# Kernel optimization log

Hardware: AMD Instinct MI355X
Metric: run time of the kernel (lower is better)

## Reference

```python
import jax, jax.numpy as jnp
import numpy as np

L, H, R, N, E = 6, 128, 64, 10000, 160000
SSILU_SCALE = 1.0 / 0.6  # ScaledSiLU
INV_SQRT_3 = 1.0 / np.sqrt(3.0)
INV_SQRT_H = 1.0 / np.sqrt(H)
INV_SQRT_2 = 1.0 / np.sqrt(2.0)


def ssilu(x):
    return jax.nn.silu(x) * SSILU_SCALE


def lnorm(x, w, b):
    m = x.mean(-1, keepdims=True)
    v = jnp.var(x, axis=-1, keepdims=True)
    return (x - m) * jax.lax.rsqrt(v + 1e-5) * w + b


def gated_block(x, v, wv1, wv2, wu1, bu1, wu2, bu2, hout):
    # GatedEquivariantBlock: x [N,Hin], v [N,3,Hin]
    vec1 = jnp.linalg.norm(jnp.einsum('nci,io->nco', v, wv1), axis=-2)  # [N,Hin]
    vec2 = jnp.einsum('nci,io->nco', v, wv2)                            # [N,3,hout]
    h = ssilu(jnp.concatenate([x, vec1], -1) @ wu1 + bu1) @ wu2 + bu2   # [N,2*hout]
    xs, xv = h[..., :hout], h[..., hout:]
    return ssilu(xs), xv[:, None, :] * vec2


def forward_impl(edge_index, x, vec, edge_rbf, edge_vector,
                 ln_w, ln_b, xp1_w, xp1_b, xp2_w, xp2_b, rbf_w, rbf_b,
                 vp_w, xv1_w, xv1_b, xv2_w, xv2_b,
                 we1, be1, we2, be2,
                 g1_v1, g1_v2, g1_u1, g1_u1b, g1_u2, g1_u2b,
                 g2_v1, g2_v2, g2_u1, g2_u1b, g2_u2, g2_u2b):
    src, dst = edge_index[0], edge_index[1]  # message flows src(j) -> dst(i)
    for l in range(L):
        # ---- PaiNNMessage ----
        xh = ssilu(lnorm(x, ln_w[l], ln_b[l]) @ xp1_w[l] + xp1_b[l]) @ xp2_w[l] + xp2_b[l]  # [N,3H]
        rbfh = edge_rbf @ rbf_w[l] + rbf_b[l]                                                # [E,3H]
        m = xh[src] * rbfh                                                                    # gather + elementwise
        mx = m[:, :H]
        m2 = m[:, H:2 * H] * INV_SQRT_3
        m3 = m[:, 2 * H:]
        mvec = (vec[src] * m2[:, None, :] + m3[:, None, :] * edge_vector[:, :, None]) * INV_SQRT_H  # [E,3,H]
        dx = jax.ops.segment_sum(mx, dst, num_segments=N)
        dvec = jax.ops.segment_sum(mvec, dst, num_segments=N)
        x = (x + dx) * INV_SQRT_2
        vec = vec + dvec
        # ---- PaiNNUpdate ----
        vp = jnp.einsum('nci,io->nco', vec, vp_w[l])  # [N,3,2H]
        v1, v2 = vp[..., :H], vp[..., H:]
        vec_dot = (v1 * v2).sum(axis=1) * INV_SQRT_H  # [N,H]
        vnorm = jnp.sqrt((v2 ** 2).sum(axis=-2) + 1e-8)
        h = ssilu(jnp.concatenate([x, vnorm], -1) @ xv1_w[l] + xv1_b[l]) @ xv2_w[l] + xv2_b[l]  # [N,3H]
        xu1, xu2, xu3 = h[:, :H], h[:, H:2 * H], h[:, 2 * H:]
        x = x + (xu1 + xu2 * vec_dot) * INV_SQRT_2
        vec = vec + xu3[:, None, :] * v1
        # ScaleFactor is identity without a scale file
    energy = ssilu(x @ we1 + be1) @ we2 + be2  # [N,1] per-atom energy
    fx, fv = gated_block(x, vec, g1_v1, g1_v2, g1_u1, g1_u1b, g1_u2, g1_u2b, H // 2)
    fx, fv = gated_block(fx, fv, g2_v1, g2_v2, g2_u1, g2_u1b, g2_u2, g2_u2b, 1)
    forces = fv[..., 0]  # [N,3]
    return jnp.concatenate([energy, forces], axis=-1)  # [N,4] packed (energy, fx, fy, fz)


def setup_inputs() -> dict:
    key = jax.random.key(0)
    ks = iter(jax.random.split(key, 64))
    nrm = lambda shape, s=0.05: jax.random.normal(next(ks), shape, jnp.float32) * s
    return dict(
        x=jax.random.normal(next(ks), (N, H), jnp.float32),
        vec=jax.random.normal(next(ks), (N, 3, H), jnp.float32),
        edge_index=jax.random.randint(next(ks), (2, E), 0, N),
        edge_rbf=jax.random.uniform(next(ks), (E, R), jnp.float32),
        edge_vector=jax.random.normal(next(ks), (E, 3), jnp.float32),
        ln_w=jnp.ones((L, H)), ln_b=jnp.zeros((L, H)),
        xp1_w=nrm((L, H, H)), xp1_b=jnp.zeros((L, H)),
        xp2_w=nrm((L, H, 3 * H)), xp2_b=jnp.zeros((L, 3 * H)),
        rbf_w=nrm((L, R, 3 * H)), rbf_b=jnp.zeros((L, 3 * H)),
        vp_w=nrm((L, H, 2 * H)),
        xv1_w=nrm((L, 2 * H, H)), xv1_b=jnp.zeros((L, H)),
        xv2_w=nrm((L, H, 3 * H)), xv2_b=jnp.zeros((L, 3 * H)),
        we1=nrm((H, H // 2)), be1=jnp.zeros((H // 2,)),
        we2=nrm((H // 2, 1)), be2=jnp.zeros((1,)),
        g1_v1=nrm((H, H)), g1_v2=nrm((H, H // 2)),
        g1_u1=nrm((2 * H, H)), g1_u1b=jnp.zeros((H,)),
        g1_u2=nrm((H, H)), g1_u2b=jnp.zeros((H,)),
        g2_v1=nrm((H // 2, H // 2)), g2_v2=nrm((H // 2, 1)),
        g2_u1=nrm((H, H // 2)), g2_u1b=jnp.zeros((H // 2,)),
        g2_u2=nrm((H // 2, 2)), g2_u2b=jnp.zeros((2,)),
    )


def reference(x, vec, edge_index, edge_rbf, edge_vector,
              ln_w, ln_b, xp1_w, xp1_b, xp2_w, xp2_b, rbf_w, rbf_b,
              vp_w, xv1_w, xv1_b, xv2_w, xv2_b,
              we1, be1, we2, be2,
              g1_v1, g1_v2, g1_u1, g1_u1b, g1_u2, g1_u2b,
              g2_v1, g2_v2, g2_u1, g2_u1b, g2_u2, g2_u2b):
    return forward_impl(edge_index, x, vec, edge_rbf, edge_vector,
                        ln_w, ln_b, xp1_w, xp1_b, xp2_w, xp2_b, rbf_w, rbf_b,
                        vp_w, xv1_w, xv1_b, xv2_w, xv2_b,
                        we1, be1, we2, be2,
                        g1_v1, g1_v2, g1_u1, g1_u1b, g1_u2, g1_u2b,
                        g2_v1, g2_v2, g2_u1, g2_u1b, g2_u2, g2_u2b)
```

## Files before the change

kernel.cpp:

```cpp
#include <hip/hip_runtime.h>
#include <hip/hip_bf16.h>

#define NN 10000
#define EE 160000
#define LL 6

#define INV_SQRT_3f  0.57735026919f
#define INV_SQRT_Hf  0.08838834764832f
#define INV_SQRT_2f  0.70710678118655f

typedef _Float16 half8 __attribute__((ext_vector_type(8)));
typedef float f32x4 __attribute__((ext_vector_type(4)));

__device__ __forceinline__ float ssilu_f(float v){
  float s = 1.0f / (1.0f + __expf(-v));
  return v * s * 1.6666666666667f;
}
__device__ __forceinline__ float bcast(float v, int l){
  return __int_as_float(__builtin_amdgcn_readlane(__float_as_int(v), l));
}

__global__ __launch_bounds__(256) void k_hist(const int* __restrict__ edst, int* __restrict__ cnt){
  int i = blockIdx.x*256 + threadIdx.x;
  if (i < EE) atomicAdd(&cnt[edst[i]], 1);
}

__global__ __launch_bounds__(1024) void k_scan(const int* __restrict__ cnt,
                                               int* __restrict__ off, int* __restrict__ cur){
  __shared__ int ps[1024];
  int t = threadIdx.x;
  int base = t*10;
  int local[10];
  int s = 0;
  #pragma unroll
  for (int i=0;i<10;i++){
    int c = (base+i < NN) ? cnt[base+i] : 0;
    local[i] = s; s += c;
  }
  ps[t] = s;
  __syncthreads();
  for (int d=1; d<1024; d<<=1){
    int v = (t>=d) ? ps[t-d] : 0;
    __syncthreads();
    ps[t] += v;
    __syncthreads();
  }
  int pre = (t>0) ? ps[t-1] : 0;
  #pragma unroll
  for (int i=0;i<10;i++){
    int idx = base+i;
    if (idx < NN){ int o = pre + local[i]; off[idx]=o; cur[idx]=o; }
  }
  if (t==1023) off[NN] = ps[1023];
}

__global__ __launch_bounds__(256) void k_fill(const int* __restrict__ edst,
                                              int* __restrict__ cur, int* __restrict__ eord){
  int i = blockIdx.x*256 + threadIdx.x;
  if (i < EE){
    int d = edst[i];
    int p = atomicAdd(&cur[d], 1);
    eord[p] = i;
  }
}

__global__ __launch_bounds__(256) void k_packw(const float* __restrict__ w, _Float16* __restrict__ wf){
  int i = blockIdx.x*256 + threadIdx.x;
  if (i >= LL*24*2*64*8) return;
  int j    = i & 7;
  int lane = (i >> 3) & 63;
  int kh   = (i >> 9) & 1;
  int rest = i >> 10;
  int nb   = rest % 24;
  int l    = rest / 24;
  int k    = 32*kh + 8*(lane>>4) + j;
  int ch   = nb*16 + (lane&15);
  float v = w[((size_t)l*64 + k)*384 + ch];
  if (ch >= 128 && ch < 256) v *= INV_SQRT_3f;
  wf[i] = (_Float16)v;
}

__global__ __launch_bounds__(256) void k_packb(const float* __restrict__ b, float* __restrict__ bsc){
  int i = blockIdx.x*256 + threadIdx.x;
  if (i >= LL*384) return;
  int ch = i % 384;
  float v = b[i];
  if (ch >= 128 && ch < 256) v *= INV_SQRT_3f;
  bsc[i] = v;
}

struct PackTab {
  const float* s[30];
  _Float16* d[30];
  int K[30];
  int NO[30];
};
__global__ __launch_bounds__(256) void k_packall(PackTab tb){
  int e = blockIdx.y;
  int K = tb.K[e], NO = tb.NO[e];
  int tot = K*NO, KS = K >> 5;
  const float* s = tb.s[e];
  _Float16* d = tb.d[e];
  for (int i = blockIdx.x*256 + threadIdx.x; i < tot; i += gridDim.x*256){
    int j = i & 7, lane = (i >> 3) & 63, rest = i >> 9;
    int ks = rest % KS, nb = rest / KS;
    int k = ks*32 + (lane>>4)*8 + j, n = nb*16 + (lane&15);
    d[i] = (_Float16)s[(size_t)k*NO + n];
  }
}

__global__ __launch_bounds__(256) void k_cvt16(const float* __restrict__ v, _Float16* __restrict__ o, int n){
  int i = blockIdx.x*256 + threadIdx.x;
  if (i < n) o[i] = (_Float16)v[i];
}

__global__ __launch_bounds__(64) void k_gemm_rbfh(
    const float* __restrict__ erbf, const _Float16* __restrict__ wf,
    const float* __restrict__ bsc, const int* __restrict__ eord,
    _Float16* __restrict__ rbfh)
{
  int lane = threadIdx.x;
  int i0 = blockIdx.x * 64;
  int ml = lane & 15, kg = lane >> 4;
  half8 a0[4], a1[4];
  #pragma unroll
  for (int tt = 0; tt < 4; tt++){
    int e_m = eord[i0 + tt*16 + ml];
    const float* ar = erbf + (size_t)e_m*64 + 8*kg;
    float4 p0 = *(const float4*)(ar);
    float4 p1 = *(const float4*)(ar+4);
    a0[tt][0]=(_Float16)p0.x; a0[tt][1]=(_Float16)p0.y; a0[tt][2]=(_Float16)p0.z; a0[tt][3]=(_Float16)p0.w;
    a0[tt][4]=(_Float16)p1.x; a0[tt][5]=(_Float16)p1.y; a0[tt][6]=(_Float16)p1.z; a0[tt][7]=(_Float16)p1.w;
    float4 p2 = *(const float4*)(ar+32);
    float4 p3 = *(const float4*)(ar+36);
    a1[tt][0]=(_Float16)p2.x; a1[tt][1]=(_Float16)p2.y; a1[tt][2]=(_Float16)p2.z; a1[tt][3]=(_Float16)p2.w;
    a1[tt][4]=(_Float16)p3.x; a1[tt][5]=(_Float16)p3.y; a1[tt][6]=(_Float16)p3.z; a1[tt][7]=(_Float16)p3.w;
  }
  #pragma unroll 2
  for (int nb = 0; nb < 24; nb++){
    half8 b0 = *(const half8*)(wf + ((size_t)(nb*2+0)*64 + lane)*8);
    half8 b1 = *(const half8*)(wf + ((size_t)(nb*2+1)*64 + lane)*8);
    float bias = bsc[nb*16 + ml];
    #pragma unroll
    for (int tt = 0; tt < 4; tt++){
      f32x4 acc = {bias, bias, bias, bias};
      acc = __builtin_amdgcn_mfma_f32_16x16x32_f16(a0[tt], b0, acc, 0, 0, 0);
      acc = __builtin_amdgcn_mfma_f32_16x16x32_f16(a1[tt], b1, acc, 0, 0, 0);
      _Float16* orow = rbfh + (size_t)(i0 + tt*16)*384 + nb*16 + ml;
      #pragma unroll
      for (int r = 0; r < 4; r++)
        orow[(size_t)(kg*4 + r)*384] = (_Float16)acc[r];
    }
  }
}

__global__ __launch_bounds__(256) void k_xh_mfma(
    const float* __restrict__ x,
    const float* __restrict__ lnw, const float* __restrict__ lnb,
    const _Float16* __restrict__ wf1, const float* __restrict__ b1,
    const _Float16* __restrict__ wf2, const float* __restrict__ b2,
    _Float16* __restrict__ xh16)
{
  __shared__ _Float16 sA[32][136];
  __shared__ _Float16 sH[32][136];
  int t = threadIdx.x;
  int n0 = blockIdx.x * 32;
  {
    int nd = t >> 3, sb = t & 7;
    int node = n0 + nd;
// ... 52 lines not shown
      int nb = (w&1)*4 + nb4;
      #pragma unroll
      for (int r = 0; r < 4; r++)
        sH[mt*16 + kg*4 + r][nb*16 + ml] = (_Float16)hout[nb4][r];
    }
  }
  __syncthreads();
  {
    half8 a[4];
    #pragma unroll
    for (int ks = 0; ks < 4; ks++)
      a[ks] = *(const half8*)&sH[mt*16 + ml][ks*32 + kg*8];
    #pragma unroll 4
    for (int nb12 = 0; nb12 < 12; nb12++){
      int nb = (w&1)*12 + nb12;
      float bias = b2[nb*16 + ml];
      f32x4 acc = {bias, bias, bias, bias};
      #pragma unroll
      for (int ks = 0; ks < 4; ks++)
        acc = __builtin_amdgcn_mfma_f32_16x16x32_f16(a[ks],
                *(const half8*)(wf2 + ((size_t)(nb*4+ks)*64 + lane)*8), acc, 0,0,0);
      #pragma unroll
      for (int r = 0; r < 4; r++){
        int m = mt*16 + kg*4 + r;
        int node = n0 + m;
        if (node < NN) xh16[(size_t)node*384 + nb*16 + ml] = (_Float16)acc[r];
      }
    }
  }
}

__global__ __launch_bounds__(256) void k_edge3(
    const _Float16* __restrict__ rbfh,
    const int* __restrict__ esrc,
    const int* __restrict__ eord, const int* __restrict__ off,
    const float* __restrict__ evec,
    const _Float16* __restrict__ xh16, const _Float16* __restrict__ vec16,
    float* __restrict__ dx, float* __restrict__ dvec)
{
  int t = threadIdx.x;
  int lane = t & 63;
  int n = blockIdx.x*4 + (t>>6);
  if (n >= NN) return;
  int o0 = off[n], o1 = off[n+1];
  float ax0 = 0.f, ax1 = 0.f;
  float av00=0.f, av01=0.f, av10=0.f, av11=0.f, av20=0.f, av21=0.f;
  #pragma unroll 2
  for (int p = o0; p < o1; p++){
    int eid = eord[p];
    const _Float16* hr = rbfh + (size_t)p*384;
    float h0 = (float)hr[lane];
    float h1 = (float)hr[64+lane];
    float h2 = (float)hr[128+lane];
    float h3 = (float)hr[192+lane];
    float h4 = (float)hr[256+lane];
    float h5 = (float)hr[320+lane];
    int sN = esrc[eid];
    const _Float16* xr = xh16 + (size_t)sN*384;
    float m0  = h0 * (float)xr[lane];
    float m1  = h1 * (float)xr[64+lane];
    float m2a = h2 * (float)xr[128+lane];
    float m2b = h3 * (float)xr[192+lane];
    float m3a = h4 * (float)xr[256+lane];
    float m3b = h5 * (float)xr[320+lane];
    ax0 += m0; ax1 += m1;
    const _Float16* vr = vec16 + (size_t)sN*384;
    float ev0 = evec[(size_t)eid*3 + 0];
    float ev1 = evec[(size_t)eid*3 + 1];
    float ev2 = evec[(size_t)eid*3 + 2];
    av00 = fmaf((float)vr[lane],     m2a, av00); av00 = fmaf(m3a, ev0, av00);
    av01 = fmaf((float)vr[64+lane],  m2b, av01); av01 = fmaf(m3b, ev0, av01);
    av10 = fmaf((float)vr[128+lane], m2a, av10); av10 = fmaf(m3a, ev1, av10);
    av11 = fmaf((float)vr[192+lane], m2b, av11); av11 = fmaf(m3b, ev1, av11);
    av20 = fmaf((float)vr[256+lane], m2a, av20); av20 = fmaf(m3a, ev2, av20);
    av21 = fmaf((float)vr[320+lane], m2b, av21); av21 = fmaf(m3b, ev2, av21);
  }
  float* dxr = dx + (size_t)n*128;
  dxr[lane] = ax0; dxr[64+lane] = ax1;
  float* dvr = dvec + (size_t)n*384;
  dvr[lane]     = av00 * INV_SQRT_Hf;
  dvr[64+lane]  = av01 * INV_SQRT_Hf;
  dvr[128+lane] = av10 * INV_SQRT_Hf;
  dvr[192+lane] = av11 * INV_SQRT_Hf;
  dvr[256+lane] = av20 * INV_SQRT_Hf;
  dvr[320+lane] = av21 * INV_SQRT_Hf;
}

__global__ __launch_bounds__(256) void k_node_mfma(
    float* __restrict__ xbuf, float* __restrict__ vbuf,
    const float* __restrict__ dx, const float* __restrict__ dvec,
    const _Float16* __restrict__ wfvp,
    const _Float16* __restrict__ wfxv1, const float* __restrict__ xv1_b,
    const _Float16* __restrict__ wfxv2, const float* __restrict__ xv2_b,
    _Float16* __restrict__ vec16)
{
  __shared__ _Float16 sV1[96][136];
  __shared__ _Float16 sCat[32][264];
  __shared__ _Float16 sVD[32][128];
  int t = threadIdx.x;
  int n0 = blockIdx.x * 32;
  int lane = t & 63, w = t >> 6, ml = lane & 15, kg = lane >> 4;
  int mt = w & 1, nbb = (w >> 1) * 4;
  float vd[4][4], vn[4][4];
  #pragma unroll
  for (int i=0;i<4;i++){
    #pragma unroll
    for (int r=0;r<4;r++){ vd[i][r]=0.f; vn[i][r]=0.f; }
  }
// ... 114 lines not shown
      #pragma unroll
      for (int ks = 0; ks < 4; ks++){
        au1 = __builtin_amdgcn_mfma_f32_16x16x32_f16(a[ks],
                *(const half8*)(wfxv2 + ((size_t)(nbu*4+ks)*64 + lane)*8), au1, 0,0,0);
        au2 = __builtin_amdgcn_mfma_f32_16x16x32_f16(a[ks],
                *(const half8*)(wfxv2 + ((size_t)((nbu+8)*4+ks)*64 + lane)*8), au2, 0,0,0);
        au3 = __builtin_amdgcn_mfma_f32_16x16x32_f16(a[ks],
                *(const half8*)(wfxv2 + ((size_t)((nbu+16)*4+ks)*64 + lane)*8), au3, 0,0,0);
      }
      #pragma unroll
      for (int r = 0; r < 4; r++){
        int m = mt*16 + kg*4 + r;
        int node = n0 + m;
        if (node >= NN) continue;
        int c = nbu*16 + ml;
        float xu1 = au1[r], xu2 = au2[r], xu3 = au3[r];
        float vdv = (float)sVD[m][c];
        size_t px = (size_t)node*128 + c;
        float xn = (xbuf[px] + dx[px]) * INV_SQRT_2f;
        xbuf[px] = xn + (xu1 + xu2*vdv) * INV_SQRT_2f;
        #pragma unroll
        for (int cd = 0; cd < 3; cd++){
          float v1v = (float)sV1[cd*32 + m][c];
          size_t pv = (size_t)node*384 + cd*128 + c;
          float vo = vbuf[pv] + dvec[pv] + xu3*v1v;
          vbuf[pv] = vo;
          vec16[pv] = (_Float16)vo;
        }
      }
    }
  }
}

__global__ __launch_bounds__(256) void k_final1(
    const float* __restrict__ x, const float* __restrict__ vec,
    const float* __restrict__ we1, const float* __restrict__ be1,
    const float* __restrict__ we2, const float* __restrict__ be2,
    const float* __restrict__ wv1, const float* __restrict__ wv2,
    const float* __restrict__ wu1, const float* __restrict__ bu1,
    const float* __restrict__ wu2, const float* __restrict__ bu2,
    float* __restrict__ out, float* __restrict__ fx, float* __restrict__ fv)
{
  __shared__ __align__(16) float s_x[8][128];
  __shared__ __align__(16) float s_vl[8][384];
  __shared__ __align__(16) float s_p[8][384];
  __shared__ __align__(16) float s_n1[8][128];
  __shared__ __align__(16) float s_v2[8][192];
  __shared__ __align__(16) float s_h[8][128];
  __shared__ __align__(16) float s_h2[8][128];
  __shared__ __align__(16) float s_e1[8][64];
  int t = threadIdx.x;
  int n0 = blockIdx.x * 8;
  for (int idx = t; idx < 8*128; idx += 256){
    int i = idx >> 7, h = idx & 127;
    s_x[i][h] = x[(size_t)(n0+i)*128 + h];
  }
  for (int idx = t; idx < 8*384; idx += 256){
    int i = idx / 384, h = idx % 384;
    s_vl[i][h] = vec[(size_t)(n0+i)*384 + h];
  }
  __syncthreads();
  {
    int c = t & 63;
    int gb = t >> 6;
    #pragma unroll
    for (int u = 0; u < 2; u++){
      int i = gb + 4*u;
      float acc = be1[c];
      for (int k = 0; k < 128; k += 4){
        float w0 = we1[(k+0)*64+c], wq = we1[(k+1)*64+c], wz = we1[(k+2)*64+c], ww = we1[(k+3)*64+c];
        float4 a = *(const float4*)&s_x[i][k];
        acc = fmaf(a.x,w0,acc); acc=fmaf(a.y,wq,acc); acc=fmaf(a.z,wz,acc); acc=fmaf(a.w,ww,acc);
      }
      s_e1[i][c] = ssilu_f(acc);
    }
  }
  __syncthreads();
  {
    int lane = t & 63;
    int gb = t >> 6;
    #pragma unroll
    for (int u = 0; u < 2; u++){
      int i = gb + 4*u;
      float v = s_e1[i][lane] * we2[lane];
      #pragma unroll
      for (int off = 32; off > 0; off >>= 1) v += __shfl_xor(v, off, 64);
      if (lane == 0) out[(size_t)(n0+i)*4 + 0] = v + be2[0];
    }
  }
  {
    int ob = t & 127;
    int ib = (t >> 7) * 4;
    float acc[4][3];
    #pragma unroll
    for (int ii=0;ii<4;ii++){
      #pragma unroll
      for (int cd=0;cd<3;cd++) acc[ii][cd]=0.f;
    }
    for (int k = 0; k < 128; k += 4){
      float w0 = wv1[(k+0)*128+ob], wq=wv1[(k+1)*128+ob], wz=wv1[(k+2)*128+ob], ww=wv1[(k+3)*128+ob];
      #pragma unroll
      for (int ii=0;ii<4;ii++){
        #pragma unroll
        for (int cd=0;cd<3;cd++){
          float4 a = *(const float4*)&s_vl[ib+ii][cd*128+k];
          float s0=acc[ii][cd];
          s0=fmaf(a.x,w0,s0); s0=fmaf(a.y,wq,s0); s0=fmaf(a.z,wz,s0); s0=fmaf(a.w,ww,s0);
          acc[ii][cd]=s0;
        }
      }
    }
    #pragma unroll
    for (int ii=0;ii<4;ii++){
      #pragma unroll
      for (int cd=0;cd<3;cd++) s_p[ib+ii][cd*128+ob] = acc[ii][cd];
    }
  }
  __syncthreads();
  #pragma unroll
  for (int rep = 0; rep < 4; rep++){
    int idx = rep*256+t;
    int i = idx >> 7, h = idx & 127;
    float p0 = s_p[i][h], p1 = s_p[i][128+h], p2 = s_p[i][256+h];
    s_n1[i][h] = sqrtf(p0*p0 + p1*p1 + p2*p2);
  }
  {
    int c = t & 63;
    int gb = t >> 6;
    float acc[2][3];
    #pragma unroll
    for (int u=0;u<2;u++){
      #pragma unroll
      for (int cd=0;cd<3;cd++) acc[u][cd]=0.f;
    }
    for (int k=0;k<128;k+=4){
      float w0=wv2[(k+0)*64+c], wq=wv2[(k+1)*64+c], wz=wv2[(k+2)*64+c], ww=wv2[(k+3)*64+c];
      #pragma unroll
      for (int u=0;u<2;u++){
        int i = gb + 4*u;
        #pragma unroll
        for (int cd=0;cd<3;cd++){
          float4 a = *(const float4*)&s_vl[i][cd*128+k];
          float s0=acc[u][cd];
          s0=fmaf(a.x,w0,s0); s0=fmaf(a.y,wq,s0); s0=fmaf(a.z,wz,s0); s0=fmaf(a.w,ww,s0);
          acc[u][cd]=s0;
        }
      }
    }
    #pragma unroll
    for (int u=0;u<2;u++){
      int i=gb+4*u;
      #pragma unroll
      for (int cd=0;cd<3;cd++) s_v2[i][cd*64+c]=acc[u][cd];
    }
  }
  __syncthreads();
  {
    int c = t & 127;
    int ib = (t >> 7) * 4;
    float acc[4];
    float bv = bu1[c];
    #pragma unroll
    for (int ii=0;ii<4;ii++) acc[ii]=bv;
    for (int k=0;k<128;k+=4){
      float w0=wu1[(k+0)*128+c], wq=wu1[(k+1)*128+c], wz=wu1[(k+2)*128+c], ww=wu1[(k+3)*128+c];
      #pragma unroll
      for (int ii=0;ii<4;ii++){
        float4 a = *(const float4*)&s_x[ib+ii][k];
        acc[ii]=fmaf(a.x,w0,acc[ii]); acc[ii]=fmaf(a.y,wq,acc[ii]); acc[ii]=fmaf(a.z,wz,acc[ii]); acc[ii]=fmaf(a.w,ww,acc[ii]);
      }
    }
    for (int k=0;k<128;k+=4){
      float w0=wu1[(128+k+0)*128+c], wq=wu1[(128+k+1)*128+c], wz=wu1[(128+k+2)*128+c], ww=wu1[(128+k+3)*128+c];
      #pragma unroll
      for (int ii=0;ii<4;ii++){
        float4 a = *(const float4*)&s_n1[ib+ii][k];
        acc[ii]=fmaf(a.x,w0,acc[ii]); acc[ii]=fmaf(a.y,wq,acc[ii]); acc[ii]=fmaf(a.z,wz,acc[ii]); acc[ii]=fmaf(a.w,ww,acc[ii]);
      }
    }
    #pragma unroll
    for (int ii=0;ii<4;ii++) s_h[ib+ii][c] = ssilu_f(acc[ii]);
  }
  __syncthreads();
  {
    int c = t & 127;
    int ib = (t >> 7) * 4;
    float acc[4];
    float bv = bu2[c];
    #pragma unroll
    for (int ii=0;ii<4;ii++) acc[ii]=bv;
    for (int k=0;k<128;k+=4){
      float w0=wu2[(k+0)*128+c], wq=wu2[(k+1)*128+c], wz=wu2[(k+2)*128+c], ww=wu2[(k+3)*128+c];
      #pragma unroll
      for (int ii=0;ii<4;ii++){
        float4 a = *(const float4*)&s_h[ib+ii][k];
        acc[ii]=fmaf(a.x,w0,acc[ii]); acc[ii]=fmaf(a.y,wq,acc[ii]); acc[ii]=fmaf(a.z,wz,acc[ii]); acc[ii]=fmaf(a.w,ww,acc[ii]);
      }
    }
    #pragma unroll
    for (int ii=0;ii<4;ii++) s_h2[ib+ii][c] = acc[ii];
  }
  __syncthreads();
  {
    int c = t & 63;
    int gb = t >> 6;
    #pragma unroll
    for (int u=0;u<2;u++){
      int i = gb + 4*u;
      fx[(size_t)(n0+i)*64 + c] = ssilu_f(s_h2[i][c]);
      float xv = s_h2[i][64+c];
      #pragma unroll
      for (int cd=0;cd<3;cd++)
        fv[(size_t)(n0+i)*192 + cd*64 + c] = xv * s_v2[i][cd*64+c];
    }
  }
}

__global__ __launch_bounds__(256) void k_final2(
    const float* __restrict__ fx, const float* __restrict__ fv,
    const float* __restrict__ wv1, const float* __restrict__ wv2,
    const float* __restrict__ wu1, const float* __restrict__ bu1,
    const float* __restrict__ wu2, const float* __restrict__ bu2,
    float* __restrict__ out)
{
  int t = threadIdx.x;
  int lane = t & 63;
  int n = blockIdx.x * 4 + (t >> 6);
  float fxv = fx[(size_t)n*64 + lane];
  float f0 = fv[(size_t)n*192 + lane];
  float f1 = fv[(size_t)n*192 + 64 + lane];
  float f2 = fv[(size_t)n*192 + 128 + lane];
  float a0=0.f, a1=0.f, a2=0.f;
  for (int k=0;k<64;k++){
    float w = wv1[k*64 + lane];
    a0 = fmaf(bcast(f0,k), w, a0);
    a1 = fmaf(bcast(f1,k), w, a1);
    a2 = fmaf(bcast(f2,k), w, a2);
  }
  float n1 = sqrtf(a0*a0 + a1*a1 + a2*a2);
  float w2v = wv2[lane];
  float r0 = f0*w2v, r1 = f1*w2v, r2 = f2*w2v;
  #pragma unroll
  for (int off=32; off>0; off>>=1){
    r0 += __shfl_xor(r0, off, 64);
    r1 += __shfl_xor(r1, off, 64);
    r2 += __shfl_xor(r2, off, 64);
  }
  float acc = bu1[lane];
  for (int k=0;k<64;k++) acc = fmaf(bcast(fxv,k), wu1[k*64+lane], acc);
  for (int k=0;k<64;k++) acc = fmaf(bcast(n1,k), wu1[(64+k)*64+lane], acc);
  float hv = ssilu_f(acc);
  float s1 = hv * wu2[lane*2 + 1];
  #pragma unroll
  for (int off=32; off>0; off>>=1) s1 += __shfl_xor(s1, off, 64);
  float h2_1 = s1 + bu2[1];
  if (lane == 0){
    out[(size_t)n*4 + 1] = h2_1 * r0;
    out[(size_t)n*4 + 2] = h2_1 * r1;
    out[(size_t)n*4 + 3] = h2_1 * r2;
  }
}

extern "C" void kernel_launch(void* const* d_in, const int* in_sizes, int n_in,
                              void* d_out, int out_size, void* d_ws, size_t ws_size,
                              hipStream_t stream)
{
  const float* x_in   = (const float*)d_in[0];
  const float* vec_in = (const float*)d_in[1];
  const int*   eidx   = (const int*)d_in[2];
  const float* erbf   = (const float*)d_in[3];
  const float* evec   = (const float*)d_in[4];
  const float* ln_w  = (const float*)d_in[5];
  const float* ln_b  = (const float*)d_in[6];
  const float* xp1_w = (const float*)d_in[7];
  const float* xp1_b = (const float*)d_in[8];
  const float* xp2_w = (const float*)d_in[9];
  const float* xp2_b = (const float*)d_in[10];
  const float* rbf_w = (const float*)d_in[11];
  const float* rbf_b = (const float*)d_in[12];
  const float* vp_w  = (const float*)d_in[13];
  const float* xv1_w = (const float*)d_in[14];
  const float* xv1_b = (const float*)d_in[15];
  const float* xv2_w = (const float*)d_in[16];
  const float* xv2_b = (const float*)d_in[17];
  const float* we1 = (const float*)d_in[18];
  const float* be1 = (const float*)d_in[19];
  const float* we2 = (const float*)d_in[20];
  const float* be2 = (const float*)d_in[21];
  const float* g1_v1 = (const float*)d_in[22];
  const float* g1_v2 = (const float*)d_in[23];
  const float* g1_u1 = (const float*)d_in[24];
  const float* g1_u1b = (const float*)d_in[25];
  const float* g1_u2 = (const float*)d_in[26];
  const float* g1_u2b = (const float*)d_in[27];
  const float* g2_v1 = (const float*)d_in[28];
  const float* g2_v2 = (const float*)d_in[29];
  const float* g2_u1 = (const float*)d_in[30];
  const float* g2_u1b = (const float*)d_in[31];
  const float* g2_u2 = (const float*)d_in[32];
  const float* g2_u2b = (const float*)d_in[33];
  float* out = (float*)d_out;

  char* base = (char*)d_ws;
  size_t o = 0;
  auto alloc = [&](size_t bytes) -> char* {
    char* p = base + o;
    o = (o + bytes + 255) & ~(size_t)255;
    return p;
  };
  float* x_cur   = (float*)alloc((size_t)NN*128*4);
  float* vec_cur = (float*)alloc((size_t)NN*384*4);
  float* dx      = (float*)alloc((size_t)NN*128*4);
  float* dvec    = (float*)alloc((size_t)NN*384*4);
  _Float16* xh16 = (_Float16*)alloc((size_t)NN*384*2);
  _Float16* vec16= (_Float16*)alloc((size_t)NN*384*2);
  int*   eord    = (int*)alloc((size_t)EE*4);
  int*   off     = (int*)alloc((size_t)(NN+1)*4);
  _Float16* wf   = (_Float16*)alloc((size_t)LL*24576*2);
  float* bsc     = (float*)alloc((size_t)LL*384*4);
  _Float16* wfn  = (_Float16*)alloc((size_t)LL*180224*2);
  _Float16* rbfh = (_Float16*)alloc((size_t)EE*384*2);
  float* fxb = dx;
  float* fvb = dvec;
  int* cnt = (int*)dx;
  int* cur = cnt + NN;

  hipMemcpyAsync(x_cur, x_in, sizeof(float)*(size_t)NN*128, hipMemcpyDeviceToDevice, stream);
  hipMemcpyAsync(vec_cur, vec_in, sizeof(float)*(size_t)NN*384, hipMemcpyDeviceToDevice, stream);

  const int* esrc = eidx;
  const int* edst = eidx + EE;

  hipMemsetAsync(cnt, 0, sizeof(int)*NN, stream);
  k_hist<<<(EE+255)/256, 256, 0, stream>>>(edst, cnt);
  k_scan<<<1, 1024, 0, stream>>>(cnt, off, cur);
  k_fill<<<(EE+255)/256, 256, 0, stream>>>(edst, cur, eord);
  k_packw<<<(LL*24576+255)/256, 256, 0, stream>>>(rbf_w, wf);
  k_packb<<<(LL*384+255)/256, 256, 0, stream>>>(rbf_b, bsc);
  k_cvt16<<<(NN*384+255)/256, 256, 0, stream>>>(vec_in, vec16, NN*384);

  {
    PackTab tb;
    for (int l = 0; l < LL; l++){
      _Float16* wb = wfn + (size_t)l*180224;
      tb.s[l*5+0] = xp1_w + (size_t)l*128*128; tb.d[l*5+0] = wb;          tb.K[l*5+0]=128; tb.NO[l*5+0]=128;
      tb.s[l*5+1] = xp2_w + (size_t)l*128*384; tb.d[l*5+1] = wb+16384;    tb.K[l*5+1]=128; tb.NO[l*5+1]=384;
      tb.s[l*5+2] = vp_w  + (size_t)l*128*256; tb.d[l*5+2] = wb+65536;    tb.K[l*5+2]=128; tb.NO[l*5+2]=256;
      tb.s[l*5+3] = xv1_w + (size_t)l*256*128; tb.d[l*5+3] = wb+98304;    tb.K[l*5+3]=256; tb.NO[l*5+3]=128;
      tb.s[l*5+4] = xv2_w + (size_t)l*128*384; tb.d[l*5+4] = wb+131072;   tb.K[l*5+4]=128; tb.NO[l*5+4]=384;
    }
    k_packall<<<dim3(24, 30), 256, 0, stream>>>(tb);
  }

  for (int l = 0; l < LL; l++){
    _Float16* wb = wfn + (size_t)l*180224;
    k_xh_mfma<<<(NN+31)/32, 256, 0, stream>>>(x_cur, ln_w + l*128, ln_b + l*128,
        wb, xp1_b + l*128, wb+16384, xp2_b + l*384, xh16);
    k_gemm_rbfh<<<EE/64, 64, 0, stream>>>(erbf, wf + (size_t)l*24576,
        bsc + (size_t)l*384, eord, rbfh);
    k_edge3<<<NN/4, 256, 0, stream>>>(rbfh, esrc, eord, off, evec, xh16, vec16, dx, dvec);
    k_node_mfma<<<(NN+31)/32, 256, 0, stream>>>(x_cur, vec_cur, dx, dvec,
        wb+65536, wb+98304, xv1_b + l*128, wb+131072, xv2_b + l*384, vec16);
  }
  k_final1<<<NN/8, 256, 0, stream>>>(x_cur, vec_cur, we1, be1, we2, be2,
      g1_v1, g1_v2, g1_u1, g1_u1b, g1_u2, g1_u2b, out, fxb, fvb);
  k_final2<<<NN/4, 256, 0, stream>>>(fxb, fvb, g2_v1, g2_v2, g2_u1, g2_u1b, g2_u2, g2_u2b, out);
}
```

Baseline: 1.085 ms.

## Pre-sort edge inputs into MFMA layout and fuse output head into one MFMA kernel

The edge RBF features are gathered once, in destination-sorted order, converted to fp16 and stored in the MFMA operand layout. The per-layer rbf GEMM then does contiguous half8 loads instead of a gathered fp32 load and conversion on every layer. Edge vectors and source indices are packed into one sorted float4 array, which removes the eord indirection in the edge aggregation loop. The two scalar fp32 output-head kernels are replaced by one fused fp16 MFMA kernel that keeps its intermediates in LDS, at the cost of fp16 precision in the head and extra workspace plus one-time sorting passes.

```diff
diff --git a/kernel.cpp b/kernel.cpp
--- a/kernel.cpp
+++ b/kernel.cpp
@@ -11,6 +11,15 @@
 
 typedef _Float16 half8 __attribute__((ext_vector_type(8)));
 typedef float f32x4 __attribute__((ext_vector_type(4)));
+
+#define WE1OFF   0
+#define WV1OFF   8192
+#define WV2OFF   24576
+#define WU1OFF   32768
+#define WU2OFF   65536
+#define G2V1OFF  81920
+#define G2U1OFF  86016
+#define WFIN_SZ  94208
 
 __device__ __forceinline__ float ssilu_f(float v){
   float s = 1.0f / (1.0f + __expf(-v));
@@ -62,6 +71,25 @@
     int p = atomicAdd(&cur[d], 1);
     eord[p] = i;
   }
+}
+
+__global__ __launch_bounds__(256) void k_sorta(const float* __restrict__ erbf,
+                                               const int* __restrict__ eord, _Float16* __restrict__ eA){
+  long i = (long)blockIdx.x*256 + threadIdx.x;
+  if (i >= (long)EE*64) return;
+  int j = i & 7, lane = (i >> 3) & 63, kh = (i >> 9) & 1;
+  long tile = i >> 10;
+  int e = eord[tile*16 + (lane&15)];
+  eA[i] = (_Float16)erbf[(size_t)e*64 + kh*32 + (lane>>4)*8 + j];
+}
+
+__global__ __launch_bounds__(256) void k_sorte(const int* __restrict__ esrc, const float* __restrict__ evec,
+                                               const int* __restrict__ eord, float4* __restrict__ es4){
+  int p = blockIdx.x*256 + threadIdx.x;
+  if (p >= EE) return;
+  int e = eord[p];
+  es4[p] = make_float4(evec[(size_t)e*3], evec[(size_t)e*3+1], evec[(size_t)e*3+2],
+                       __int_as_float(esrc[e]));
 }
 
 __global__ __launch_bounds__(256) void k_packw(const float* __restrict__ w, _Float16* __restrict__ wf){
@@ -90,10 +118,10 @@
 }
 
 struct PackTab {
-  const float* s[30];
-  _Float16* d[30];
-  int K[30];
-  int NO[30];
+  const float* s[40];
+  _Float16* d[40];
+  int K[40];
+  int NO[40];
 };
 __global__ __launch_bounds__(256) void k_packall(PackTab tb){
   int e = blockIdx.y;
@@ -115,26 +143,19 @@
 }
 
 __global__ __launch_bounds__(64) void k_gemm_rbfh(
-    const float* __restrict__ erbf, const _Float16* __restrict__ wf,
-    const float* __restrict__ bsc, const int* __restrict__ eord,
+    const _Float16* __restrict__ eA, const _Float16* __restrict__ wf,
+    const float* __restrict__ bsc,
     _Float16* __restrict__ rbfh)
 {
   int lane = threadIdx.x;
   int i0 = blockIdx.x * 64;
+  int tg = blockIdx.x * 4;
   int ml = lane & 15, kg = lane >> 4;
   half8 a0[4], a1[4];
   #pragma unroll
   for (int tt = 0; tt < 4; tt++){
-    int e_m = eord[i0 + tt*16 + ml];
-    const float* ar = erbf + (size_t)e_m*64 + 8*kg;
-    float4 p0 = *(const float4*)(ar);
-    float4 p1 = *(const float4*)(ar+4);
-    a0[tt][0]=(_Float16)p0.x; a0[tt][1]=(_Float16)p0.y; a0[tt][2]=(_Float16)p0.z; a0[tt][3]=(_Float16)p0.w;
-    a0[tt][4]=(_Float16)p1.x; a0[tt][5]=(_Float16)p1.y; a0[tt][6]=(_Float16)p1.z; a0[tt][7]=(_Float16)p1.w;
-    float4 p2 = *(const float4*)(ar+32);
-    float4 p3 = *(const float4*)(ar+36);
-    a1[tt][0]=(_Float16)p2.x; a1[tt][1]=(_Float16)p2.y; a1[tt][2]=(_Float16)p2.z; a1[tt][3]=(_Float16)p2.w;
-    a1[tt][4]=(_Float16)p3.x; a1[tt][5]=(_Float16)p3.y; a1[tt][6]=(_Float16)p3.z; a1[tt][7]=(_Float16)p3.w;
+    a0[tt] = *(const half8*)(eA + ((size_t)((tg+tt)*2+0)*64 + lane)*8);
+    a1[tt] = *(const half8*)(eA + ((size_t)((tg+tt)*2+1)*64 + lane)*8);
   }
   #pragma unroll 2
   for (int nb = 0; nb < 24; nb++){
@@ -253,9 +274,7 @@
 
 __global__ __launch_bounds__(256) void k_edge3(
     const _Float16* __restrict__ rbfh,
-    const int* __restrict__ esrc,
-    const int* __restrict__ eord, const int* __restrict__ off,
-    const float* __restrict__ evec,
+    const float4* __restrict__ es4, const int* __restrict__ off,
     const _Float16* __restrict__ xh16, const _Float16* __restrict__ vec16,
     float* __restrict__ dx, float* __restrict__ dvec)
 {
@@ -268,7 +287,6 @@
   float av00=0.f, av01=0.f, av10=0.f, av11=0.f, av20=0.f, av21=0.f;
   #pragma unroll 2
   for (int p = o0; p < o1; p++){
-    int eid = eord[p];
     const _Float16* hr = rbfh + (size_t)p*384;
     float h0 = (float)hr[lane];
     float h1 = (float)hr[64+lane];
@@ -276,7 +294,8 @@
     float h3 = (float)hr[192+lane];
     float h4 = (float)hr[256+lane];
     float h5 = (float)hr[320+lane];
-    int sN = esrc[eid];
+    float4 q = es4[p];
+    int sN = __float_as_int(q.w);
     const _Float16* xr = xh16 + (size_t)sN*384;
     float m0  = h0 * (float)xr[lane];
     float m1  = h1 * (float)xr[64+lane];
@@ -286,15 +305,12 @@
     float m3b = h5 * (float)xr[320+lane];
     ax0 += m0; ax1 += m1;
     const _Float16* vr = vec16 + (size_t)sN*384;
-    float ev0 = evec[(size_t)eid*3 + 0];
-    float ev1 = evec[(size_t)eid*3 + 1];
-    float ev2 = evec[(size_t)eid*3 + 2];
-    av00 = fmaf((float)vr[lane],     m2a, av00); av00 = fmaf(m3a, ev0, av00);
-    av01 = fmaf((float)vr[64+lane],  m2b, av01); av01 = fmaf(m3b, ev0, av01);
-    av10 = fmaf((float)vr[128+lane], m2a, av10); av10 = fmaf(m3a, ev1, av10);
-    av11 = fmaf((float)vr[192+lane], m2b, av11); av11 = fmaf(m3b, ev1, av11);
-    av20 = fmaf((float)vr[256+lane], m2a, av20); av20 = fmaf(m3a, ev2, av20);
-    av21 = fmaf((float)vr[320+lane], m2b, av21); av21 = fmaf(m3b, ev2, av21);
+    av00 = fmaf((float)vr[lane],     m2a, av00); av00 = fmaf(m3a, q.x, av00);
+    av01 = fmaf((float)vr[64+lane],  m2b, av01); av01 = fmaf(m3b, q.x, av01);
+    av10 = fmaf((float)vr[128+lane], m2a, av10); av10 = fmaf(m3a, q.y, av10);
+    av11 = fmaf((float)vr[192+lane], m2b, av11); av11 = fmaf(m3b, q.y, av11);
+    av20 = fmaf((float)vr[256+lane], m2a, av20); av20 = fmaf(m3a, q.z, av20);
+    av21 = fmaf((float)vr[320+lane], m2b, av21); av21 = fmaf(m3b, q.z, av21);
   }
   float* dxr = dx + (size_t)n*128;
   dxr[lane] = ax0; dxr[64+lane] = ax1;
@@ -475,232 +491,251 @@
   }
 }
 
-__global__ __launch_bounds__(256) void k_final1(
+__global__ __launch_bounds__(256) void k_final(
     const float* __restrict__ x, const float* __restrict__ vec,
-    const float* __restrict__ we1, const float* __restrict__ be1,
-    const float* __restrict__ we2, const float* __restrict__ be2,
-    const float* __restrict__ wv1, const float* __restrict__ wv2,
-    const float* __restrict__ wu1, const float* __restrict__ bu1,
-    const float* __restrict__ wu2, const float* __restrict__ bu2,
-    float* __restrict__ out, float* __restrict__ fx, float* __restrict__ fv)
-{
-  __shared__ __align__(16) float s_x[8][128];
-  __shared__ __align__(16) float s_vl[8][384];
-  __shared__ __align__(16) float s_p[8][384];
-  __shared__ __align__(16) float s_n1[8][128];
-  __shared__ __align__(16) float s_v2[8][192];
-  __shared__ __align__(16) float s_h[8][128];
-  __shared__ __align__(16) float s_h2[8][128];
-  __shared__ __align__(16) float s_e1[8][64];
-  int t = threadIdx.x;
-  int n0 = blockIdx.x * 8;
-  for (int idx = t; idx < 8*128; idx += 256){
-    int i = idx >> 7, h = idx & 127;
-    s_x[i][h] = x[(size_t)(n0+i)*128 + h];
-  }
-  for (int idx = t; idx < 8*384; idx += 256){
-    int i = idx / 384, h = idx % 384;
-    s_vl[i][h] = vec[(size_t)(n0+i)*384 + h];
-  }
-  __syncthreads();
-  {
-    int c = t & 63;
-    int gb = t >> 6;
-    #pragma unroll
-    for (int u = 0; u < 2; u++){
-      int i = gb + 4*u;
-      float acc = be1[c];
-      for (int k = 0; k < 128; k += 4){
-        float w0 = we1[(k+0)*64+c], wq = we1[(k+1)*64+c], wz = we1[(k+2)*64+c], ww = we1[(k+3)*64+c];
-        float4 a = *(const float4*)&s_x[i][k];
-        acc = fmaf(a.x,w0,acc); acc=fmaf(a.y,wq,acc); acc=fmaf(a.z,wz,acc); acc=fmaf(a.w,ww,acc);
-      }
-      s_e1[i][c] = ssilu_f(acc);
-    }
-  }
-  __syncthreads();
-  {
-    int lane = t & 63;
-    int gb = t >> 6;
-    #pragma unroll
-    for (int u = 0; u < 2; u++){
-      int i = gb + 4*u;
-      float v = s_e1[i][lane] * we2[lane];
-      #pragma unroll
-      for (int off = 32; off > 0; off >>= 1) v += __shfl_xor(v, off, 64);
-      if (lane == 0) out[(size_t)(n0+i)*4 + 0] = v + be2[0];
-    }
-  }
-  {
-    int ob = t & 127;
-    int ib = (t >> 7) * 4;
-    float acc[4][3];
-    #pragma unroll
-    for (int ii=0;ii<4;ii++){
-      #pragma unroll
-      for (int cd=0;cd<3;cd++) acc[ii][cd]=0.f;
-    }
-    for (int k = 0; k < 128; k += 4){
-      float w0 = wv1[(k+0)*128+ob], wq=wv1[(k+1)*128+ob], wz=wv1[(k+2)*128+ob], ww=wv1[(k+3)*128+ob];
-      #pragma unroll
-      for (int ii=0;ii<4;ii++){
-        #pragma unroll
-        for (int cd=0;cd<3;cd++){
-          float4 a = *(const float4*)&s_vl[ib+ii][cd*128+k];
-          float s0=acc[ii][cd];
-          s0=fmaf(a.x,w0,s0); s0=fmaf(a.y,wq,s0); s0=fmaf(a.z,wz,s0); s0=fmaf(a.w,ww,s0);
-          acc[ii][cd]=s0;
-        }
-      }
-    }
-    #pragma unroll
-    for (int ii=0;ii<4;ii++){
-      #pragma unroll
-      for (int cd=0;cd<3;cd++) s_p[ib+ii][cd*128+ob] = acc[ii][cd];
-    }
-  }
-  __syncthreads();
-  #pragma unroll
-  for (int rep = 0; rep < 4; rep++){
-    int idx = rep*256+t;
-    int i = idx >> 7, h = idx & 127;
-    float p0 = s_p[i][h], p1 = s_p[i][128+h], p2 = s_p[i][256+h];
-    s_n1[i][h] = sqrtf(p0*p0 + p1*p1 + p2*p2);
-  }
-  {
-    int c = t & 63;
-    int gb = t >> 6;
-    float acc[2][3];
-    #pragma unroll
-    for (int u=0;u<2;u++){
-      #pragma unroll
-      for (int cd=0;cd<3;cd++) acc[u][cd]=0.f;
-    }
-    for (int k=0;k<128;k+=4){
-      float w0=wv2[(k+0)*64+c], wq=wv2[(k+1)*64+c], wz=wv2[(k+2)*64+c], ww=wv2[(k+3)*64+c];
-      #pragma unroll
-      for (int u=0;u<2;u++){
-        int i = gb + 4*u;
-        #pragma unroll
-        for (int cd=0;cd<3;cd++){
-          float4 a = *(const float4*)&s_vl[i][cd*128+k];
-          float s0=acc[u][cd];
-          s0=fmaf(a.x,w0,s0); s0=fmaf(a.y,wq,s0); s0=fmaf(a.z,wz,s0); s0=fmaf(a.w,ww,s0);
-          acc[u][cd]=s0;
-        }
-      }
-    }
-    #pragma unroll
-    for (int u=0;u<2;u++){
-      int i=gb+4*u;
-      #pragma unroll
-      for (int cd=0;cd<3;cd++) s_v2[i][cd*64+c]=acc[u][cd];
-    }
-  }
-  __syncthreads();
-  {
-    int c = t & 127;
-    int ib = (t >> 7) * 4;
-    float acc[4];
-    float bv = bu1[c];
-    #pragma unroll
-    for (int ii=0;ii<4;ii++) acc[ii]=bv;
-    for (int k=0;k<128;k+=4){
-      float w0=wu1[(k+0)*128+c], wq=wu1[(k+1)*128+c], wz=wu1[(k+2)*128+c], ww=wu1[(k+3)*128+c];
-      #pragma unroll
-      for (int ii=0;ii<4;ii++){
-        float4 a = *(const float4*)&s_x[ib+ii][k];
-        acc[ii]=fmaf(a.x,w0,acc[ii]); acc[ii]=fmaf(a.y,wq,acc[ii]); acc[ii]=fmaf(a.z,wz,acc[ii]); acc[ii]=fmaf(a.w,ww,acc[ii]);
-      }
-    }
-    for (int k=0;k<128;k+=4){
-      float w0=wu1[(128+k+0)*128+c], wq=wu1[(128+k+1)*128+c], wz=wu1[(128+k+2)*128+c], ww=wu1[(128+k+3)*128+c];
-      #pragma unroll
-      for (int ii=0;ii<4;ii++){
-        float4 a = *(const float4*)&s_n1[ib+ii][k];
-        acc[ii]=fmaf(a.x,w0,acc[ii]); acc[ii]=fmaf(a.y,wq,acc[ii]); acc[ii]=fmaf(a.z,wz,acc[ii]); acc[ii]=fmaf(a.w,ww,acc[ii]);
-      }
-    }
-    #pragma unroll
-    for (int ii=0;ii<4;ii++) s_h[ib+ii][c] = ssilu_f(acc[ii]);
-  }
-  __syncthreads();
-  {
-    int c = t & 127;
-    int ib = (t >> 7) * 4;
-    float acc[4];
-    float bv = bu2[c];
-    #pragma unroll
-    for (int ii=0;ii<4;ii++) acc[ii]=bv;
-    for (int k=0;k<128;k+=4){
-      float w0=wu2[(k+0)*128+c], wq=wu2[(k+1)*128+c], wz=wu2[(k+2)*128+c], ww=wu2[(k+3)*128+c];
-      #pragma unroll
-      for (int ii=0;ii<4;ii++){
-        float4 a = *(const float4*)&s_h[ib+ii][k];
-        acc[ii]=fmaf(a.x,w0,acc[ii]); acc[ii]=fmaf(a.y,wq,acc[ii]); acc[ii]=fmaf(a.z,wz,acc[ii]); acc[ii]=fmaf(a.w,ww,acc[ii]);
-      }
-    }
-    #pragma unroll
-    for (int ii=0;ii<4;ii++) s_h2[ib+ii][c] = acc[ii];
-  }
-  __syncthreads();
-  {
-    int c = t & 63;
-    int gb = t >> 6;
-    #pragma unroll
-    for (int u=0;u<2;u++){
-      int i = gb + 4*u;
-      fx[(size_t)(n0+i)*64 + c] = ssilu_f(s_h2[i][c]);
-      float xv = s_h2[i][64+c];
-      #pragma unroll
-      for (int cd=0;cd<3;cd++)
-        fv[(size_t)(n0+i)*192 + cd*64 + c] = xv * s_v2[i][cd*64+c];
-    }
-  }
-}
-
-__global__ __launch_bounds__(256) void k_final2(
-    const float* __restrict__ fx, const float* __restrict__ fv,
-    const float* __restrict__ wv1, const float* __restrict__ wv2,
-    const float* __restrict__ wu1, const float* __restrict__ bu1,
-    const float* __restrict__ wu2, const float* __restrict__ bu2,
+    const _Float16* __restrict__ wfin,
+    const float* __restrict__ be1, const float* __restrict__ we2, const float* __restrict__ be2,
+    const float* __restrict__ u1b, const float* __restrict__ u2b,
+    const float* __restrict__ g2v2, const float* __restrict__ g2u1b, const float* __restrict__ g2u2,
+    const float* __restrict__ g2u2b,
     float* __restrict__ out)
 {
+  __shared__ _Float16 sCat[32][264];
+  __shared__ _Float16 sV2[3][32][72];
+  __shared__ _Float16 sH[32][136];
+  __shared__ _Float16 sFV[3][32][72];
+  __shared__ _Float16 sE1[32][72];
+  __shared__ float sR[3][32];
   int t = threadIdx.x;
-  int lane = t & 63;
-  int n = blockIdx.x * 4 + (t >> 6);
-  float fxv = fx[(size_t)n*64 + lane];
-  float f0 = fv[(size_t)n*192 + lane];
-  float f1 = fv[(size_t)n*192 + 64 + lane];
-  float f2 = fv[(size_t)n*192 + 128 + lane];
-  float a0=0.f, a1=0.f, a2=0.f;
-  for (int k=0;k<64;k++){
-    float w = wv1[k*64 + lane];
-    a0 = fmaf(bcast(f0,k), w, a0);
-    a1 = fmaf(bcast(f1,k), w, a1);
-    a2 = fmaf(bcast(f2,k), w, a2);
-  }
-  float n1 = sqrtf(a0*a0 + a1*a1 + a2*a2);
-  float w2v = wv2[lane];
-  float r0 = f0*w2v, r1 = f1*w2v, r2 = f2*w2v;
-  #pragma unroll
-  for (int off=32; off>0; off>>=1){
-    r0 += __shfl_xor(r0, off, 64);
-    r1 += __shfl_xor(r1, off, 64);
-    r2 += __shfl_xor(r2, off, 64);
-  }
-  float acc = bu1[lane];
-  for (int k=0;k<64;k++) acc = fmaf(bcast(fxv,k), wu1[k*64+lane], acc);
-  for (int k=0;k<64;k++) acc = fmaf(bcast(n1,k), wu1[(64+k)*64+lane], acc);
-  float hv = ssilu_f(acc);
-  float s1 = hv * wu2[lane*2 + 1];
-  #pragma unroll
-  for (int off=32; off>0; off>>=1) s1 += __shfl_xor(s1, off, 64);
-  float h2_1 = s1 + bu2[1];
-  if (lane == 0){
-    out[(size_t)n*4 + 1] = h2_1 * r0;
-    out[(size_t)n*4 + 2] = h2_1 * r1;
-    out[(size_t)n*4 + 3] = h2_1 * r2;
+  int n0 = blockIdx.x * 32;
+  int lane = t & 63, w = t >> 6, ml = lane & 15, kg = lane >> 4;
+  int mt = w & 1, nh = w >> 1;
+
+  {
+    int nd = t >> 3, sb = t & 7;
+    int node = n0 + nd;
+    if (node < NN){
+      const float* xr = x + (size_t)node*128 + sb*16;
+      #pragma unroll
+      for (int g = 0; g < 4; g++){
+        float4 q = *(const float4*)(xr + g*4);
+        sCat[nd][sb*16+g*4+0]=(_Float16)q.x; sCat[nd][sb*16+g*4+1]=(_Float16)q.y;
+        sCat[nd][sb*16+g*4+2]=(_Float16)q.z; sCat[nd][sb*16+g*4+3]=(_Float16)q.w;
+      }
+    } else {
+      #pragma unroll
+      for (int u = 0; u < 16; u++) sCat[nd][sb*16+u] = (_Float16)0.f;
+    }
+  }
+  {
+    int arow = n0 + mt*16 + ml;
+    bool aok = arow < NN;
+    float n1sq[4][4];
+    #pragma unroll
+    for (int i=0;i<4;i++){
+      #pragma unroll
+      for (int r=0;r<4;r++) n1sq[i][r]=0.f;
+    }
+    for (int cd = 0; cd < 3; cd++){
+      half8 a[4];
+      #pragma unroll
+      for (int ks = 0; ks < 4; ks++){
+        if (aok){
+          const float* vr = vec + (size_t)arow*384 + cd*128 + ks*32 + kg*8;
+          float4 q0 = *(const float4*)(vr);
+          float4 q1 = *(const float4*)(vr+4);
+          a[ks][0]=(_Float16)q0.x; a[ks][1]=(_Float16)q0.y; a[ks][2]=(_Float16)q0.z; a[ks][3]=(_Float16)q0.w;
+          a[ks][4]=(_Float16)q1.x; a[ks][5]=(_Float16)q1.y; a[ks][6]=(_Float16)q1.z; a[ks][7]=(_Float16)q1.w;
+        } else {
+          #pragma unroll
+          for (int j=0;j<8;j++) a[ks][j] = (_Float16)0.f;
+        }
+      }
+      #pragma unroll
+      for (int nb4 = 0; nb4 < 4; nb4++){
+        int nb = nh*4 + nb4;
+        f32x4 acc = {0.f,0.f,0.f,0.f};
+        #pragma unroll
+        for (int ks = 0; ks < 4; ks++)
+          acc = __builtin_amdgcn_mfma_f32_16x16x32_f16(a[ks],
+                  *(const half8*)(wfin + WV1OFF + ((size_t)(nb*4+ks)*64 + lane)*8), acc, 0,0,0);
+        #pragma unroll
+        for (int r = 0; r < 4; r++) n1sq[nb4][r] += acc[r]*acc[r];
+      }
+      #pragma unroll
+      for (int q = 0; q < 2; q++){
+        int nb = nh*2 + q;
+        f32x4 acc = {0.f,0.f,0.f,0.f};
+        #pragma unroll
+        for (int ks = 0; ks < 4; ks++)
+          acc = __builtin_amdgcn_mfma_f32_16x16x32_f16(a[ks],
+                  *(const half8*)(wfin + WV2OFF + ((size_t)(nb*4+ks)*64 + lane)*8), acc, 0,0,0);
+        #pragma unroll
+        for (int r = 0; r < 4; r++)
+          sV2[cd][mt*16 + kg*4 + r][nb*16 + ml] = (_Float16)acc[r];
+      }
+    }
+    #pragma unroll
+    for (int nb4 = 0; nb4 < 4; nb4++){
+      #pragma unroll
+      for (int r = 0; r < 4; r++)
+        sCat[mt*16 + kg*4 + r][128 + nh*64 + nb4*16 + ml] = (_Float16)sqrtf(n1sq[nb4][r]);
+    }
+  }
+  __syncthreads();
+  {
+    half8 a[8];
+    #pragma unroll
+    for (int ks = 0; ks < 8; ks++)
+      a[ks] = *(const half8*)&sCat[mt*16 + ml][ks*32 + kg*8];
+    #pragma unroll
+    for (int q = 0; q < 2; q++){
+      int nb = nh*2 + q;
+      float bias = be1[nb*16 + ml];
+      f32x4 acc = {bias, bias, bias, bias};
+      #pragma unroll
+      for (int ks = 0; ks < 4; ks++)
+        acc = __builtin_amdgcn_mfma_f32_16x16x32_f16(a[ks],
+                *(const half8*)(wfin + WE1OFF + ((size_t)(nb*4+ks)*64 + lane)*8), acc, 0,0,0);
+      #pragma unroll
+      for (int r = 0; r < 4; r++)
+        sE1[mt*16 + kg*4 + r][nb*16 + ml] = (_Float16)ssilu_f(acc[r]);
+    }
+    #pragma unroll
+    for (int nb4 = 0; nb4 < 4; nb4++){
+      int nb = nh*4 + nb4;
+      float bias = u1b[nb*16 + ml];
+      f32x4 acc = {bias, bias, bias, bias};
+      #pragma unroll
+      for (int ks = 0; ks < 8; ks++)
+        acc = __builtin_amdgcn_mfma_f32_16x16x32_f16(a[ks],
+                *(const half8*)(wfin + WU1OFF + ((size_t)(nb*8+ks)*64 + lane)*8), acc, 0,0,0);
+      #pragma unroll
+      for (int r = 0; r < 4; r++)
+        sH[mt*16 + kg*4 + r][nb*16 + ml] = (_Float16)ssilu_f(acc[r]);
+    }
+  }
+  __syncthreads();
+  {
+    half8 a[4];
+    #pragma unroll
+    for (int ks = 0; ks < 4; ks++)
+      a[ks] = *(const half8*)&sH[mt*16 + ml][ks*32 + kg*8];
+    #pragma unroll
+    for (int nb4 = 0; nb4 < 4; nb4++){
+      int nb = nh*4 + nb4;
+      float bias = u2b[nb*16 + ml];
+      f32x4 acc = {bias, bias, bias, bias};
+      #pragma unroll
+      for (int ks = 0; ks < 4; ks++)
+        acc = __builtin_amdgcn_mfma_f32_16x16x32_f16(a[ks],
+                *(const half8*)(wfin + WU2OFF + ((size_t)(nb*4+ks)*64 + lane)*8), acc, 0,0,0);
+      int c = nb*16 + ml;
+      #pragma unroll
+      for (int r = 0; r < 4; r++){
+        int m = mt*16 + kg*4 + r;
+        if (c < 64){
+          sCat[m][c] = (_Float16)ssilu_f(acc[r]);
+        } else {
+          float xv = acc[r];
+          #pragma unroll
+          for (int cd = 0; cd < 3; cd++)
+            sFV[cd][m][c-64] = (_Float16)(xv * (float)sV2[cd][m][c-64]);
+        }
+      }
+    }
+    float wev = we2[lane];
+    #pragma unroll
+    for (int i = 0; i < 8; i++){
+      int nd = w*8 + i;
+      float v = (float)sE1[nd][lane] * wev;
+      #pragma unroll
+      for (int o2 = 32; o2 > 0; o2 >>= 1) v += __shfl_xor(v, o2, 64);
+      int node = n0 + nd;
+      if (lane == 0 && node < NN) out[(size_t)node*4 + 0] = v + be2[0];
+    }
+  }
+  __syncthreads();
+  {
+    float n1sq[2][4];
+    #pragma unroll
+    for (int q=0;q<2;q++){
+      #pragma unroll
+      for (int r=0;r<4;r++) n1sq[q][r]=0.f;
+    }
+    for (int cd = 0; cd < 3; cd++){
+      half8 a[2];
+      #pragma unroll
+      for (int ks = 0; ks < 2; ks++)
+        a[ks] = *(const half8*)&sFV[cd][mt*16 + ml][ks*32 + kg*8];
+      #pragma unroll
+      for (int q = 0; q < 2; q++){
+        int nb = nh*2 + q;
+        f32x4 acc = {0.f,0.f,0.f,0.f};
+        #pragma unroll
+        for (int ks = 0; ks < 2; ks++)
+          acc = __builtin_amdgcn_mfma_f32_16x16x32_f16(a[ks],
+                  *(const half8*)(wfin + G2V1OFF + ((size_t)(nb*2+ks)*64 + lane)*8), acc, 0,0,0);
+        #pragma unroll
+        for (int r = 0; r < 4; r++) n1sq[q][r] += acc[r]*acc[r];
+      }
+    }
+    #pragma unroll
+    for (int q = 0; q < 2; q++){
+      #pragma unroll
+      for (int r = 0; r < 4; r++)
+        sCat[mt*16 + kg*4 + r][64 + (nh*2+q)*16 + ml] = (_Float16)sqrtf(n1sq[q][r]);
+    }
+    float g2v = g2v2[lane];
+    #pragma unroll
+    for (int i = 0; i < 8; i++){
+      int nd = w*8 + i;
+      #pragma unroll
+      for (int cd = 0; cd < 3; cd++){
+        float v = (float)sFV[cd][nd][lane] * g2v;
+        #pragma unroll
+        for (int o2 = 32; o2 > 0; o2 >>= 1) v += __shfl_xor(v, o2, 64);
+        if (lane == 0) sR[cd][nd] = v;
+      }
+    }
+  }
+  __syncthreads();
+  {
+    half8 a[4];
+    #pragma unroll
+    for (int ks = 0; ks < 4; ks++)
+      a[ks] = *(const half8*)&sCat[mt*16 + ml][ks*32 + kg*8];
+    #pragma unroll
+    for (int q = 0; q < 2; q++){
+      int nb = nh*2 + q;
+      float bias = g2u1b[nb*16 + ml];
+      f32x4 acc = {bias, bias, bias, bias};
+      #pragma unroll
+      for (int ks = 0; ks < 4; ks++)
+        acc = __builtin_amdgcn_mfma_f32_16x16x32_f16(a[ks],
+                *(const half8*)(wfin + G2U1OFF + ((size_t)(nb*4+ks)*64 + lane)*8), acc, 0,0,0);
+      #pragma unroll
+      for (int r = 0; r < 4; r++)
+        sE1[mt*16 + kg*4 + r][nb*16 + ml] = (_Float16)ssilu_f(acc[r]);
+    }
+  }
+  __syncthreads();
+  {
+    float g2w = g2u2[lane*2 + 1];
+    #pragma unroll
+    for (int i = 0; i < 8; i++){
+      int nd = w*8 + i;
+      float v = (float)sE1[nd][lane] * g2w;
+      #pragma unroll
+      for (int o2 = 32; o2 > 0; o2 >>= 1) v += __shfl_xor(v, o2, 64);
+      int node = n0 + nd;
+      if (lane == 0 && node < NN){
+        float h21 = v + g2u2b[1];
+        out[(size_t)node*4 + 1] = h21 * sR[0][nd];
+        out[(size_t)node*4 + 2] = h21 * sR[1][nd];
+        out[(size_t)node*4 + 3] = h21 * sR[2][nd];
+      }
+    }
   }
 }
 
@@ -762,9 +797,10 @@
   _Float16* wf   = (_Float16*)alloc((size_t)LL*24576*2);
   float* bsc     = (float*)alloc((size_t)LL*384*4);
   _Float16* wfn  = (_Float16*)alloc((size_t)LL*180224*2);
+  _Float16* wfin = (_Float16*)alloc((size_t)WFIN_SZ*2);
+  _Float16* eA   = (_Float16*)alloc((size_t)EE*64*2);
+  float4* es4    = (float4*)alloc((size_t)EE*16);
   _Float16* rbfh = (_Float16*)alloc((size_t)EE*384*2);
-  float* fxb = dx;
-  float* fvb = dvec;
   int* cnt = (int*)dx;
   int* cur = cnt + NN;
 
@@ -778,6 +814,8 @@
   k_hist<<<(EE+255)/256, 256, 0, stream>>>(edst, cnt);
   k_scan<<<1, 1024, 0, stream>>>(cnt, off, cur);
   k_fill<<<(EE+255)/256, 256, 0, stream>>>(edst, cur, eord);
+  k_sorta<<<(EE*64+255)/256, 256, 0, stream>>>(erbf, eord, eA);
+  k_sorte<<<(EE+255)/256, 256, 0, stream>>>(esrc, evec, eord, es4);
   k_packw<<<(LL*24576+255)/256, 256, 0, stream>>>(rbf_w, wf);
   k_packb<<<(LL*384+255)/256, 256, 0, stream>>>(rbf_b, bsc);
   k_cvt16<<<(NN*384+255)/256, 256, 0, stream>>>(vec_in, vec16, NN*384);
@@ -792,20 +830,26 @@
       tb.s[l*5+3] = xv1_w + (size_t)l*256*128; tb.d[l*5+3] = wb+98304;    tb.K[l*5+3]=256; tb.NO[l*5+3]=128;
       tb.s[l*5+4] = xv2_w + (size_t)l*128*384; tb.d[l*5+4] = wb+131072;   tb.K[l*5+4]=128; tb.NO[l*5+4]=384;
     }
-    k_packall<<<dim3(24, 30), 256, 0, stream>>>(tb);
+    tb.s[30] = we1;   tb.d[30] = wfin + WE1OFF;  tb.K[30]=128; tb.NO[30]=64;
+    tb.s[31] = g1_v1; tb.d[31] = wfin + WV1OFF;  tb.K[31]=128; tb.NO[31]=128;
+    tb.s[32] = g1_v2; tb.d[32] = wfin + WV2OFF;  tb.K[32]=128; tb.NO[32]=64;
+    tb.s[33] = g1_u1; tb.d[33] = wfin + WU1OFF;  tb.K[33]=256; tb.NO[33]=128;
+    tb.s[34] = g1_u2; tb.d[34] = wfin + WU2OFF;  tb.K[34]=128; tb.NO[34]=128;
+    tb.s[35] = g2_v1; tb.d[35] = wfin + G2V1OFF; tb.K[35]=64;  tb.NO[35]=64;
+    tb.s[36] = g2_u1; tb.d[36] = wfin + G2U1OFF; tb.K[36]=128; tb.NO[36]=64;
+    k_packall<<<dim3(24, 37), 256, 0, stream>>>(tb);
   }
 
   for (int l = 0; l < LL; l++){
     _Float16* wb = wfn + (size_t)l*180224;
     k_xh_mfma<<<(NN+31)/32, 256, 0, stream>>>(x_cur, ln_w + l*128, ln_b + l*128,
         wb, xp1_b + l*128, wb+16384, xp2_b + l*384, xh16);
-    k_gemm_rbfh<<<EE/64, 64, 0, stream>>>(erbf, wf + (size_t)l*24576,
-        bsc + (size_t)l*384, eord, rbfh);
-    k_edge3<<<NN/4, 256, 0, stream>>>(rbfh, esrc, eord, off, evec, xh16, vec16, dx, dvec);
+    k_gemm_rbfh<<<EE/64, 64, 0, stream>>>(eA, wf + (size_t)l*24576,
+        bsc + (size_t)l*384, rbfh);
+    k_edge3<<<NN/4, 256, 0, stream>>>(rbfh, es4, off, xh16, vec16, dx, dvec);
     k_node_mfma<<<(NN+31)/32, 256, 0, stream>>>(x_cur, vec_cur, dx, dvec,
         wb+65536, wb+98304, xv1_b + l*128, wb+131072, xv2_b + l*384, vec16);
   }
-  k_final1<<<NN/8, 256, 0, stream>>>(x_cur, vec_cur, we1, be1, we2, be2,
-      g1_v1, g1_v2, g1_u1, g1_u1b, g1_u2, g1_u2b, out, fxb, fvb);
-  k_final2<<<NN/4, 256, 0, stream>>>(fxb, fvb, g2_v1, g2_v2, g2_u1, g2_u1b, g2_u2, g2_u2b, out);
-}
+  k_final<<<(NN+31)/32, 256, 0, stream>>>(x_cur, vec_cur, wfin,
+      be1, we2, be2, g1_u1b, g1_u2b, g2_v2, g2_u1b, g2_u2, g2_u2b, out);
+}
```

After: 972.6 us. -10.4%, faster.
